# Optimization experiments

Measured on AMD Instinct MI355X. Metric: run time of the kernel, lower is better.

## Reference

```python
import jax, jax.numpy as jnp
import numpy as np

HEADS = 4
BN_EPS = 1e-5


def _linear_attention(x, heads):
    # x: [B, L, C]; per-head linear attention: softmax(Q,dim=feat) @ (softmax(K,dim=seq)^T @ V)
    B, L, C = x.shape
    dh = C // heads
    h = x.reshape(B, L, heads, dh)
    q = jax.nn.softmax(h, axis=-1)          # softmax over feature dim (dim=2 in torch)
    k = jax.nn.softmax(h, axis=1)           # softmax over sequence dim (dim=1 in torch)
    kv = jnp.einsum('blhd,blhe->bhde', k, h)   # [B, H, dh, dh]
    out = jnp.einsum('blhd,bhde->blhe', q, kv) # [B, L, H, dh]
    return out.reshape(B, L, C)


def setup_inputs() -> dict:
    key = jax.random.key(0)
    ks = jax.random.split(key, 10)
    B, C, L, DOUT, NB = 32, 32, 16384, 10, 3
    s = 0.1
    return {
        'x': jax.random.normal(ks[0], (B, C, L), jnp.float32),
        'fcW1': jax.random.normal(ks[1], (NB, C, C), jnp.float32) * s,
        'fcb1': jax.random.normal(ks[2], (NB, C), jnp.float32) * s,
        'fcW2': jax.random.normal(ks[3], (NB, C, C), jnp.float32) * s,
        'fcb2': jax.random.normal(ks[4], (NB, C), jnp.float32) * s,
        'Wh': jax.random.normal(ks[5], (C, C), jnp.float32) * s,
        'bh': jax.random.normal(ks[6], (C,), jnp.float32) * s,
        'bn_gamma': jnp.ones((C,), jnp.float32),
        'bn_beta': jnp.zeros((C,), jnp.float32),
        'bn_mean': jnp.zeros((C,), jnp.float32),
        'bn_var': jnp.ones((C,), jnp.float32),
        'Wf': jax.random.normal(ks[7], (C, DOUT), jnp.float32) * s,
        'bf': jax.random.normal(ks[8], (DOUT,), jnp.float32) * s,
    }


def reference(x, fcW1, fcb1, fcW2, fcb2, Wh, bh, bn_gamma, bn_beta, bn_mean, bn_var, Wf, bf):
    gelu = lambda t: jax.nn.gelu(t, approximate=False)  # torch default GELU is exact erf
    h = jnp.transpose(x, (0, 2, 1))  # [B, C, L] -> [B, L, C]
    n_blocks = fcW1.shape[0]
    for i in range(n_blocks):
        h = _linear_attention(h, HEADS)
        h = gelu(h @ fcW1[i] + fcb1[i])
        h = gelu(h @ fcW2[i] + fcb2[i])
    pooled = jnp.mean(h, axis=1)  # AdaptiveAvgPool1d(1) over L -> [B, C]
    y = pooled @ Wh + bh
    y = (y - bn_mean) * jax.lax.rsqrt(bn_var + BN_EPS) * bn_gamma + bn_beta  # BatchNorm1d (eval)
    y = gelu(y)
    return y @ Wf + bf
```

## Files before the change

### kernel.cpp

```cpp
#include <hip/hip_runtime.h>
#include <cstddef>

#define B_ 32
#define C_ 32
#define L_ 16384
#define H_ 4
#define DH_ 8
#define NB_ 3
#define DOUT_ 10
#define SEG_ 512
#define S_ (L_/SEG_)

#define TILE 256
#define AST  40
#define OST  260

typedef _Float16 f16_t;
typedef _Float16 f16x2 __attribute__((ext_vector_type(2)));
typedef _Float16 f16x8 __attribute__((ext_vector_type(8)));
typedef float    f32x4 __attribute__((ext_vector_type(4)));

__device__ __forceinline__ float gelu_f(float x){
    const float z  = fabsf(x) * 0.70710678118654752440f;
    const float t  = __builtin_amdgcn_rcpf(fmaf(0.3275911f, z, 1.0f));
    const float e  = __expf(-z * z);
    float p = fmaf(t, 1.061405429f, -1.453152027f);
    p = fmaf(t, p, 1.421413741f);
    p = fmaf(t, p, -0.284496736f);
    p = fmaf(t, p, 0.254829592f);
    const float erfz = 1.0f - p * t * e;
    const float phi  = fmaf(copysignf(erfz, x), 0.5f, 0.5f);
    return x * phi;
}

#define RED_MAX32(v) do{ v = fmaxf(v, __shfl_xor(v,1));  v = fmaxf(v, __shfl_xor(v,2)); \
                         v = fmaxf(v, __shfl_xor(v,4));  v = fmaxf(v, __shfl_xor(v,8)); \
                         v = fmaxf(v, __shfl_xor(v,16)); }while(0)
#define RED_SUM32(v) do{ v += __shfl_xor(v,1);  v += __shfl_xor(v,2); \
                         v += __shfl_xor(v,4);  v += __shfl_xor(v,8); \
                         v += __shfl_xor(v,16); }while(0)

__global__ __launch_bounds__(256) void stats_kernel(const float* __restrict__ h,
                                                    float* __restrict__ part){
    const int seg = blockIdx.x;
    const int hd  = blockIdx.y;
    const int b   = blockIdx.z;
    const int t   = threadIdx.x;
    const int d   = t >> 5;
    const int j   = t & 31;

    __shared__ float tile[8][SEG_];
    __shared__ float sm[8];

    const float* hb = h + (size_t)b * ((size_t)C_*L_) + (size_t)(hd*DH_)*L_ + (size_t)seg*SEG_;

    for (int f = t; f < 8*SEG_/4; f += 256){
        const int row = f >> 7;
        const int c4  = (f & 127) << 2;
        *(f32x4*)&tile[row][c4] = *(const f32x4*)&hb[(size_t)row*L_ + c4];
    }
    __syncthreads();

    float m = -INFINITY;
    #pragma unroll
    for (int i = 0; i < SEG_/32; i++) m = fmaxf(m, tile[d][j + 32*i]);
    RED_MAX32(m);
    if (j == 0) sm[d] = m;
    const float m_d = m;

    float s = 0.0f;
    float kv[8];
    #pragma unroll
    for (int e = 0; e < 8; e++) kv[e] = 0.0f;
    #pragma unroll
    for (int i = 0; i < SEG_/32; i++){
        const int k = j + 32*i;
        const float ek = __expf(tile[d][k] - m_d);
        s += ek;
        #pragma unroll
        for (int e = 0; e < 8; e++) kv[e] = fmaf(ek, tile[e][k], kv[e]);
    }
    RED_SUM32(s);
    #pragma unroll
    for (int e = 0; e < 8; e++){ RED_SUM32(kv[e]); }
    __syncthreads();

    float* po = part + (size_t)((b*H_ + hd)*S_ + seg) * 80;
    if (j == 0){
        po[8 + d] = s;
        #pragma unroll
        for (int e = 0; e < 8; e++) po[16 + d*8 + e] = kv[e];
    }
    if (t < 8) po[t] = sm[t];
}

template<bool LAST>
__global__ __launch_bounds__(256)
__attribute__((amdgpu_waves_per_eu(3, 4)))
void block_kernel(const float* hin,
                  float* hout,
                  const float* __restrict__ part,
                  const float* __restrict__ W1,
                  const float* __restrict__ b1,
                  const float* __restrict__ W2,
                  const float* __restrict__ b2,
                  float* __restrict__ pooled){
    __shared__ __align__(16) char AObuf[TILE*AST*2];
    f16_t* const Ash = (f16_t*)AObuf;
    float* const O16 = (float*)AObuf;
    __shared__ f16_t Bsh1[32*AST];
    __shared__ f16_t Bsh2[32*AST];
    __shared__ float sb1[32], sb2[32];
    __shared__ float kvsh[256];
    __shared__ float pool[32];

    const int tid = threadIdx.x;
    const int b   = blockIdx.y;
    const int l0  = blockIdx.x * TILE;
    const int l   = l0 + tid;
    const size_t base = (size_t)b * ((size_t)C_*L_);

    float h[32];
    #pragma unroll
    for (int c = 0; c < 32; c++) h[c] = hin[base + (size_t)c*L_ + l];

    for (int i = tid; i < 1024; i += 256){
        const int k = i >> 5, n = i & 31;
        Bsh1[n*AST + k] = (f16_t)W1[i];
        Bsh2[n*AST + k] = (f16_t)W2[i];
    }
    if (tid < 32){ sb1[tid] = b1[tid]; sb2[tid] = b2[tid]; }
    if (LAST && tid < 32) pool[tid] = 0.0f;

    {
        const int hh_t = tid >> 6;
        const int tt   = tid & 63;
        const int dd   = tt >> 3;
        const float* pp = part + (size_t)(b*H_ + hh_t) * S_ * 80;
        float M = -INFINITY;
        for (int s2 = 0; s2 < S_; s2++) M = fmaxf(M, pp[s2*80 + dd]);
        float ssum = 0.0f, kvs = 0.0f;
        for (int s2 = 0; s2 < S_; s2++){
            const float sc = __expf(pp[s2*80 + dd] - M);
            ssum = fmaf(pp[s2*80 + 8  + dd], sc, ssum);
            kvs  = fmaf(pp[s2*80 + 16 + tt], sc, kvs);
        }
        kvsh[tid] = kvs / ssum;
    }
    __syncthreads();

    float attn[32];
    #pragma unroll
    for (int hh = 0; hh < 4; hh++){
        float mq = h[hh*8];
        #pragma unroll
        for (int d2 = 1; d2 < 8; d2++) mq = fmaxf(mq, h[hh*8 + d2]);
        float es[8]; float qs = 0.f;
        #pragma unroll
        for (int d2 = 0; d2 < 8; d2++){ es[d2] = __expf(h[hh*8 + d2] - mq); qs += es[d2]; }
        const float inv = __builtin_amdgcn_rcpf(qs);
        #pragma unroll
        for (int e = 0; e < 8; e++){
            float a = 0.f;
            #pragma unroll
            for (int d2 = 0; d2 < 8; d2++) a += es[d2] * kvsh[hh*64 + d2*8 + e];
            attn[hh*8 + e] = a * inv;
        }
    }

    #pragma unroll
    for (int k2 = 0; k2 < 32; k2 += 2){
        f16x2 pr = { (f16_t)attn[k2], (f16_t)attn[k2+1] };
        *(f16x2*)&Ash[tid*AST + k2] = pr;
    }
    __syncthreads();

    const int wv   = tid >> 6;
    const int lane = tid & 63;
    const int lr   = lane & 15;
    const int lk   = lane >> 4;
    const f32x4 zero = {0.f, 0.f, 0.f, 0.f};

    f16x8 a[4], bw[2];
    f32x4 d[8];

    #pragma unroll
    for (int mt = 0; mt < 4; mt++)
        a[mt] = *(const f16x8*)&Ash[(wv*64 + mt*16 + lr)*AST + lk*8];
    #pragma unroll
    for (int nt = 0; nt < 2; nt++)
        bw[nt] = *(const f16x8*)&Bsh1[(nt*16 + lr)*AST + lk*8];
    #pragma unroll
    for (int nt = 0; nt < 2; nt++)
        #pragma unroll
        for (int mt = 0; mt < 4; mt++)
            d[nt*4+mt] = __builtin_amdgcn_mfma_f32_16x16x32_f16(a[mt], bw[nt], zero, 0, 0, 0);

    #pragma unroll
    for (int nt = 0; nt < 2; nt++){
        const float bias = sb1[nt*16 + lr];
        #pragma unroll
        for (int mt = 0; mt < 4; mt++){
            #pragma unroll
            for (int r = 0; r < 4; r++){
                const float v = gelu_f(d[nt*4+mt][r] + bias);
                Ash[(wv*64 + mt*16 + lk*4 + r)*AST + (nt*16 + lr)] = (f16_t)v;
            }
        }
    }
    __syncthreads();

    #pragma unroll
    for (int mt = 0; mt < 4; mt++)
        a[mt] = *(const f16x8*)&Ash[(wv*64 + mt*16 + lr)*AST + lk*8];
    #pragma unroll
    for (int nt = 0; nt < 2; nt++)
        bw[nt] = *(const f16x8*)&Bsh2[(nt*16 + lr)*AST + lk*8];
    #pragma unroll
    for (int nt = 0; nt < 2; nt++)
        #pragma unroll
        for (int mt = 0; mt < 4; mt++)
            d[nt*4+mt] = __builtin_amdgcn_mfma_f32_16x16x32_f16(a[mt], bw[nt], zero, 0, 0, 0);

    #pragma unroll
    for (int nt = 0; nt < 2; nt++){
        const float bias = sb2[nt*16 + lr];
        #pragma unroll
        for (int mt = 0; mt < 4; mt++)
            #pragma unroll
            for (int r = 0; r < 4; r++)
                d[nt*4+mt][r] = gelu_f(d[nt*4+mt][r] + bias);
    }

    if (!LAST){
        #pragma unroll
        for (int nt = 0; nt < 2; nt++){
            __syncthreads();
            #pragma unroll
            for (int mt = 0; mt < 4; mt++)
                *(f32x4*)&O16[lr*OST + wv*64 + mt*16 + lk*4] = d[nt*4+mt];
            __syncthreads();
            #pragma unroll
            for (int c = 0; c < 16; c++)
                hout[base + (size_t)(nt*16 + c)*L_ + l0 + tid] = O16[c*OST + tid];
        }
    } else {
        __syncthreads();
        #pragma unroll
        for (int nt = 0; nt < 2; nt++){
            float ps = 0.f;
            #pragma unroll
            for (int mt = 0; mt < 4; mt++)
                ps += d[nt*4+mt][0] + d[nt*4+mt][1] + d[nt*4+mt][2] + d[nt*4+mt][3];
            atomicAdd(&pool[nt*16 + lr], ps);
        }
        __syncthreads();
        if (tid < 32) atomicAdd(&pooled[b*32 + tid], pool[tid]);
    }
}

__global__ __launch_bounds__(1024) void head_kernel(const float* __restrict__ pooled,
                                                    const float* __restrict__ Wh,
                                                    const float* __restrict__ bh,
                                                    const float* __restrict__ gam,
                                                    const float* __restrict__ bet,
                                                    const float* __restrict__ mean,
                                                    const float* __restrict__ var,
                                                    const float* __restrict__ Wf,
                                                    const float* __restrict__ bf,
                                                    float* __restrict__ out){
    __shared__ float y2[32][32];
    const int t = threadIdx.x;
    const int b = t >> 5, c = t & 31;
    float a = bh[c];
    const float invL = 1.0f / (float)L_;
    #pragma unroll
    for (int d = 0; d < 32; d++) a += (pooled[b*32 + d] * invL) * Wh[d*32 + c];
    a = (a - mean[c]) * rsqrtf(var[c] + 1e-5f) * gam[c] + bet[c];
    y2[b][c] = gelu_f(a);
    __syncthreads();
    if (t < B_*DOUT_){
        const int b2 = t / DOUT_, j = t % DOUT_;
        float r = bf[j];
        #pragma unroll
        for (int c2 = 0; c2 < 32; c2++) r += y2[b2][c2] * Wf[c2*DOUT_ + j];
        out[t] = r;
    }
}

extern "C" void kernel_launch(void* const* d_in, const int* in_sizes, int n_in,
                              void* d_out, int out_size, void* d_ws, size_t ws_size,
                              hipStream_t stream){
    (void)in_sizes; (void)n_in; (void)out_size; (void)ws_size;
    const float* x    = (const float*)d_in[0];
    const float* fW1  = (const float*)d_in[1];
    const float* fb1  = (const float*)d_in[2];
    const float* fW2  = (const float*)d_in[3];
    const float* fb2  = (const float*)d_in[4];
    const float* Wh   = (const float*)d_in[5];
    const float* bh   = (const float*)d_in[6];
    const float* gam  = (const float*)d_in[7];
    const float* bet  = (const float*)d_in[8];
    const float* mean = (const float*)d_in[9];
    const float* var  = (const float*)d_in[10];
    const float* Wf   = (const float*)d_in[11];
    const float* bf   = (const float*)d_in[12];
    float* out = (float*)d_out;

    float* hbuf   = (float*)d_ws;
    float* part   = hbuf + (size_t)B_*C_*L_;
    float* pooled = part + (size_t)B_*H_*S_*80;

    hipMemsetAsync(pooled, 0, B_*C_*sizeof(float), stream);

    dim3 sgrid(S_, H_, B_);
    dim3 bgrid(L_/TILE, B_);

    stats_kernel<<<sgrid, 256, 0, stream>>>(x, part);
    block_kernel<false><<<bgrid, 256, 0, stream>>>(x, hbuf, part,
        fW1, fb1, fW2, fb2, nullptr);
    stats_kernel<<<sgrid, 256, 0, stream>>>(hbuf, part);
    block_kernel<false><<<bgrid, 256, 0, stream>>>(hbuf, hbuf, part,
        fW1 + C_*C_, fb1 + C_, fW2 + C_*C_, fb2 + C_, nullptr);
    stats_kernel<<<sgrid, 256, 0, stream>>>(hbuf, part);
    block_kernel<true><<<bgrid, 256, 0, stream>>>(hbuf, nullptr, part,
        fW1 + 2*C_*C_, fb1 + 2*C_, fW2 + 2*C_*C_, fb2 + 2*C_, pooled);

    head_kernel<<<1, 1024, 0, stream>>>(pooled, Wh, bh, gam, bet, mean, var, Wf, bf, out);
}
```

Baseline: 294.1 us.

## Process two sub-tiles per block, store MFMA output directly, fuse head into last block

Each block now covers 512 sequence positions as two 256-wide sub-tiles, with both input slices loaded into registers up front so the second load overlaps the first sub-tile's compute. The output no longer goes through an LDS transpose: 16-byte vectors are written straight from the MFMA accumulators to global memory. The separate head kernel is folded into the last block kernel, using a global completion counter and threadfences so the final block computes the head. This saves a launch and several barriers, but raises register pressure and makes the global stores less coalesced.

```diff
diff --git a/kernel.cpp b/kernel.cpp
--- a/kernel.cpp
+++ b/kernel.cpp
@@ -11,9 +11,8 @@
 #define SEG_ 512
 #define S_ (L_/SEG_)
 
-#define TILE 256
+#define WTILE 512
 #define AST  40
-#define OST  260
 
 typedef _Float16 f16_t;
 typedef _Float16 f16x2 __attribute__((ext_vector_type(2)));
@@ -104,25 +103,35 @@
                   const float* __restrict__ b1,
                   const float* __restrict__ W2,
                   const float* __restrict__ b2,
-                  float* __restrict__ pooled){
-    __shared__ __align__(16) char AObuf[TILE*AST*2];
-    f16_t* const Ash = (f16_t*)AObuf;
-    float* const O16 = (float*)AObuf;
+                  float* pooled,
+                  unsigned* done_ctr,
+                  const float* __restrict__ Wh,
+                  const float* __restrict__ bh,
+                  const float* __restrict__ gam,
+                  const float* __restrict__ bet,
+                  const float* __restrict__ mean,
+                  const float* __restrict__ var,
+                  const float* __restrict__ Wf,
+                  const float* __restrict__ bf,
+                  float* __restrict__ out){
+    __shared__ __align__(16) f16_t Ash[256*AST];
     __shared__ f16_t Bsh1[32*AST];
     __shared__ f16_t Bsh2[32*AST];
     __shared__ float sb1[32], sb2[32];
     __shared__ float kvsh[256];
     __shared__ float pool[32];
+    __shared__ unsigned lastf;
 
     const int tid = threadIdx.x;
     const int b   = blockIdx.y;
-    const int l0  = blockIdx.x * TILE;
-    const int l   = l0 + tid;
+    const int l0  = blockIdx.x * WTILE;
     const size_t base = (size_t)b * ((size_t)C_*L_);
 
-    float h[32];
-    #pragma unroll
-    for (int c = 0; c < 32; c++) h[c] = hin[base + (size_t)c*L_ + l];
+    float h0[32], h1[32];
+    #pragma unroll
+    for (int c = 0; c < 32; c++) h0[c] = hin[base + (size_t)c*L_ + l0 + tid];
+    #pragma unroll
+    for (int c = 0; c < 32; c++) h1[c] = hin[base + (size_t)c*L_ + l0 + 256 + tid];
 
     for (int i = tid; i < 1024; i += 256){
         const int k = i >> 5, n = i & 31;
@@ -149,142 +158,148 @@
     }
     __syncthreads();
 
-    float attn[32];
-    #pragma unroll
-    for (int hh = 0; hh < 4; hh++){
-        float mq = h[hh*8];
-        #pragma unroll
-        for (int d2 = 1; d2 < 8; d2++) mq = fmaxf(mq, h[hh*8 + d2]);
-        float es[8]; float qs = 0.f;
-        #pragma unroll
-        for (int d2 = 0; d2 < 8; d2++){ es[d2] = __expf(h[hh*8 + d2] - mq); qs += es[d2]; }
-        const float inv = __builtin_amdgcn_rcpf(qs);
-        #pragma unroll
-        for (int e = 0; e < 8; e++){
-            float a = 0.f;
-            #pragma unroll
-            for (int d2 = 0; d2 < 8; d2++) a += es[d2] * kvsh[hh*64 + d2*8 + e];
-            attn[hh*8 + e] = a * inv;
-        }
-    }
-
-    #pragma unroll
-    for (int k2 = 0; k2 < 32; k2 += 2){
-        f16x2 pr = { (f16_t)attn[k2], (f16_t)attn[k2+1] };
-        *(f16x2*)&Ash[tid*AST + k2] = pr;
-    }
-    __syncthreads();
-
     const int wv   = tid >> 6;
     const int lane = tid & 63;
     const int lr   = lane & 15;
     const int lk   = lane >> 4;
     const f32x4 zero = {0.f, 0.f, 0.f, 0.f};
 
-    f16x8 a[4], bw[2];
-    f32x4 d[8];
-
-    #pragma unroll
-    for (int mt = 0; mt < 4; mt++)
-        a[mt] = *(const f16x8*)&Ash[(wv*64 + mt*16 + lr)*AST + lk*8];
-    #pragma unroll
-    for (int nt = 0; nt < 2; nt++)
-        bw[nt] = *(const f16x8*)&Bsh1[(nt*16 + lr)*AST + lk*8];
-    #pragma unroll
-    for (int nt = 0; nt < 2; nt++)
+    auto attn_to_ash = [&](const float (&hh)[32], const bool preb){
+        float attn[32];
+        #pragma unroll
+        for (int hd2 = 0; hd2 < 4; hd2++){
+            float mq = hh[hd2*8];
+            #pragma unroll
+            for (int d2 = 1; d2 < 8; d2++) mq = fmaxf(mq, hh[hd2*8 + d2]);
+            float es[8]; float qs = 0.f;
+            #pragma unroll
+            for (int d2 = 0; d2 < 8; d2++){ es[d2] = __expf(hh[hd2*8 + d2] - mq); qs += es[d2]; }
+            const float inv = __builtin_amdgcn_rcpf(qs);
+            #pragma unroll
+            for (int e = 0; e < 8; e++){
+                float acc = 0.f;
+                #pragma unroll
+                for (int d2 = 0; d2 < 8; d2++) acc += es[d2] * kvsh[hd2*64 + d2*8 + e];
+                attn[hd2*8 + e] = acc * inv;
+            }
+        }
+        if (preb) __syncthreads();
+        #pragma unroll
+        for (int k2 = 0; k2 < 32; k2 += 2){
+            f16x2 pr = { (f16_t)attn[k2], (f16_t)attn[k2+1] };
+            *(f16x2*)&Ash[tid*AST + k2] = pr;
+        }
+    };
+
+    auto fc_and_out = [&](const int lofs){
+        f16x8 a[4], bw[2];
+        f32x4 d[8];
         #pragma unroll
         for (int mt = 0; mt < 4; mt++)
-            d[nt*4+mt] = __builtin_amdgcn_mfma_f32_16x16x32_f16(a[mt], bw[nt], zero, 0, 0, 0);
-
-    #pragma unroll
-    for (int nt = 0; nt < 2; nt++){
-        const float bias = sb1[nt*16 + lr];
-        #pragma unroll
-        for (int mt = 0; mt < 4; mt++){
-            #pragma unroll
-            for (int r = 0; r < 4; r++){
-                const float v = gelu_f(d[nt*4+mt][r] + bias);
-                Ash[(wv*64 + mt*16 + lk*4 + r)*AST + (nt*16 + lr)] = (f16_t)v;
+            a[mt] = *(const f16x8*)&Ash[(wv*64 + mt*16 + lr)*AST + lk*8];
+        #pragma unroll
+        for (int nt = 0; nt < 2; nt++)
+            bw[nt] = *(const f16x8*)&Bsh1[(nt*16 + lr)*AST + lk*8];
+        #pragma unroll
+        for (int nt = 0; nt < 2; nt++)
+            #pragma unroll
+            for (int mt = 0; mt < 4; mt++)
+                d[nt*4+mt] = __builtin_amdgcn_mfma_f32_16x16x32_f16(a[mt], bw[nt], zero, 0, 0, 0);
+
+        #pragma unroll
+        for (int nt = 0; nt < 2; nt++){
+            const float bias = sb1[nt*16 + lr];
+            #pragma unroll
+            for (int mt = 0; mt < 4; mt++)
+                #pragma unroll
+                for (int r = 0; r < 4; r++){
+                    const float v = gelu_f(d[nt*4+mt][r] + bias);
+                    Ash[(wv*64 + mt*16 + lk*4 + r)*AST + (nt*16 + lr)] = (f16_t)v;
+                }
+        }
+
+        #pragma unroll
+        for (int mt = 0; mt < 4; mt++)
+            a[mt] = *(const f16x8*)&Ash[(wv*64 + mt*16 + lr)*AST + lk*8];
+        #pragma unroll
+        for (int nt = 0; nt < 2; nt++)
+            bw[nt] = *(const f16x8*)&Bsh2[(nt*16 + lr)*AST + lk*8];
+        #pragma unroll
+        for (int nt = 0; nt < 2; nt++)
+            #pragma unroll
+            for (int mt = 0; mt < 4; mt++)
+                d[nt*4+mt] = __builtin_amdgcn_mfma_f32_16x16x32_f16(a[mt], bw[nt], zero, 0, 0, 0);
+
+        #pragma unroll
+        for (int nt = 0; nt < 2; nt++){
+            const float bias = sb2[nt*16 + lr];
+            #pragma unroll
+            for (int mt = 0; mt < 4; mt++)
+                #pragma unroll
+                for (int r = 0; r < 4; r++)
+                    d[nt*4+mt][r] = gelu_f(d[nt*4+mt][r] + bias);
+        }
+
+        if (!LAST){
+            #pragma unroll
+            for (int nt = 0; nt < 2; nt++)
+                #pragma unroll
+                for (int mt = 0; mt < 4; mt++)
+                    *(f32x4*)&hout[base + (size_t)(nt*16 + lr)*L_
+                                   + l0 + lofs + wv*64 + mt*16 + lk*4] = d[nt*4+mt];
+        } else {
+            #pragma unroll
+            for (int nt = 0; nt < 2; nt++){
+                float ps = 0.f;
+                #pragma unroll
+                for (int mt = 0; mt < 4; mt++)
+                    ps += d[nt*4+mt][0] + d[nt*4+mt][1] + d[nt*4+mt][2] + d[nt*4+mt][3];
+                atomicAdd(&pool[nt*16 + lr], ps);
             }
         }
-    }
-    __syncthreads();
-
-    #pragma unroll
-    for (int mt = 0; mt < 4; mt++)
-        a[mt] = *(const f16x8*)&Ash[(wv*64 + mt*16 + lr)*AST + lk*8];
-    #pragma unroll
-    for (int nt = 0; nt < 2; nt++)
-        bw[nt] = *(const f16x8*)&Bsh2[(nt*16 + lr)*AST + lk*8];
-    #pragma unroll
-    for (int nt = 0; nt < 2; nt++)
-        #pragma unroll
-        for (int mt = 0; mt < 4; mt++)
-            d[nt*4+mt] = __builtin_amdgcn_mfma_f32_16x16x32_f16(a[mt], bw[nt], zero, 0, 0, 0);
-
-    #pragma unroll
-    for (int nt = 0; nt < 2; nt++){
-        const float bias = sb2[nt*16 + lr];
-        #pragma unroll
-        for (int mt = 0; mt < 4; mt++)
-            #pragma unroll
-            for (int r = 0; r < 4; r++)
-                d[nt*4+mt][r] = gelu_f(d[nt*4+mt][r] + bias);
-    }
-
-    if (!LAST){
-        #pragma unroll
-        for (int nt = 0; nt < 2; nt++){
+    };
+
+    attn_to_ash(h0, false);
+    __syncthreads();
+    fc_and_out(0);
+    attn_to_ash(h1, true);
+    __syncthreads();
+    fc_and_out(256);
+
+    if (LAST){
+        __syncthreads();
+        if (tid < 32){
+            atomicAdd(&pooled[b*32 + tid], pool[tid]);
+            __threadfence();
+        }
+        __syncthreads();
+        if (tid == 0){
+            const unsigned old = atomicAdd(done_ctr, 1u);
+            lastf = (old == 1023u) ? 1u : 0u;
+        }
+        __syncthreads();
+        if (lastf){
+            __threadfence();
+            float* y2 = (float*)Ash;
+            const float invL = 1.0f / (float)L_;
+            for (int i = tid; i < 1024; i += 256){
+                const int bb = i >> 5, cc = i & 31;
+                float acc = bh[cc];
+                #pragma unroll
+                for (int dd2 = 0; dd2 < 32; dd2++)
+                    acc += (pooled[bb*32 + dd2] * invL) * Wh[dd2*32 + cc];
+                acc = (acc - mean[cc]) * rsqrtf(var[cc] + 1e-5f) * gam[cc] + bet[cc];
+                y2[i] = gelu_f(acc);
+            }
             __syncthreads();
-            #pragma unroll
-            for (int mt = 0; mt < 4; mt++)
-                *(f32x4*)&O16[lr*OST + wv*64 + mt*16 + lk*4] = d[nt*4+mt];
-            __syncthreads();
-            #pragma unroll
-            for (int c = 0; c < 16; c++)
-                hout[base + (size_t)(nt*16 + c)*L_ + l0 + tid] = O16[c*OST + tid];
-        }
-    } else {
-        __syncthreads();
-        #pragma unroll
-        for (int nt = 0; nt < 2; nt++){
-            float ps = 0.f;
-            #pragma unroll
-            for (int mt = 0; mt < 4; mt++)
-                ps += d[nt*4+mt][0] + d[nt*4+mt][1] + d[nt*4+mt][2] + d[nt*4+mt][3];
-            atomicAdd(&pool[nt*16 + lr], ps);
-        }
-        __syncthreads();
-        if (tid < 32) atomicAdd(&pooled[b*32 + tid], pool[tid]);
-    }
-}
-
-__global__ __launch_bounds__(1024) void head_kernel(const float* __restrict__ pooled,
-                                                    const float* __restrict__ Wh,
-                                                    const float* __restrict__ bh,
-                                                    const float* __restrict__ gam,
-                                                    const float* __restrict__ bet,
-                                                    const float* __restrict__ mean,
-                                                    const float* __restrict__ var,
-                                                    const float* __restrict__ Wf,
-                                                    const float* __restrict__ bf,
-                                                    float* __restrict__ out){
-    __shared__ float y2[32][32];
-    const int t = threadIdx.x;
-    const int b = t >> 5, c = t & 31;
-    float a = bh[c];
-    const float invL = 1.0f / (float)L_;
-    #pragma unroll
-    for (int d = 0; d < 32; d++) a += (pooled[b*32 + d] * invL) * Wh[d*32 + c];
-    a = (a - mean[c]) * rsqrtf(var[c] + 1e-5f) * gam[c] + bet[c];
-    y2[b][c] = gelu_f(a);
-    __syncthreads();
-    if (t < B_*DOUT_){
-        const int b2 = t / DOUT_, j = t % DOUT_;
-        float r = bf[j];
-        #pragma unroll
-        for (int c2 = 0; c2 < 32; c2++) r += y2[b2][c2] * Wf[c2*DOUT_ + j];
-        out[t] = r;
+            for (int i = tid; i < B_*DOUT_; i += 256){
+                const int b2 = i / DOUT_, j = i % DOUT_;
+                float r = bf[j];
+                #pragma unroll
+                for (int c2 = 0; c2 < 32; c2++) r += y2[b2*32 + c2] * Wf[c2*DOUT_ + j];
+                out[i] = r;
+            }
+        }
     }
 }
 
@@ -307,24 +322,26 @@
     const float* bf   = (const float*)d_in[12];
     float* out = (float*)d_out;
 
-    float* hbuf   = (float*)d_ws;
-    float* part   = hbuf + (size_t)B_*C_*L_;
-    float* pooled = part + (size_t)B_*H_*S_*80;
-
-    hipMemsetAsync(pooled, 0, B_*C_*sizeof(float), stream);
+    float* hbuf    = (float*)d_ws;
+    float* part    = hbuf + (size_t)B_*C_*L_;
+    float* pooled  = part + (size_t)B_*H_*S_*80;
+    unsigned* done = (unsigned*)(pooled + B_*C_);
+
+    hipMemsetAsync(pooled, 0, (B_*C_ + 1)*sizeof(float), stream);
 
     dim3 sgrid(S_, H_, B_);
-    dim3 bgrid(L_/TILE, B_);
+    dim3 bgrid(L_/WTILE, B_);
 
     stats_kernel<<<sgrid, 256, 0, stream>>>(x, part);
     block_kernel<false><<<bgrid, 256, 0, stream>>>(x, hbuf, part,
-        fW1, fb1, fW2, fb2, nullptr);
+        fW1, fb1, fW2, fb2, nullptr, nullptr,
+        nullptr, nullptr, nullptr, nullptr, nullptr, nullptr, nullptr, nullptr, nullptr);
     stats_kernel<<<sgrid, 256, 0, stream>>>(hbuf, part);
     block_kernel<false><<<bgrid, 256, 0, stream>>>(hbuf, hbuf, part,
-        fW1 + C_*C_, fb1 + C_, fW2 + C_*C_, fb2 + C_, nullptr);
+        fW1 + C_*C_, fb1 + C_, fW2 + C_*C_, fb2 + C_, nullptr, nullptr,
+        nullptr, nullptr, nullptr, nullptr, nullptr, nullptr, nullptr, nullptr, nullptr);
     stats_kernel<<<sgrid, 256, 0, stream>>>(hbuf, part);
     block_kernel<true><<<bgrid, 256, 0, stream>>>(hbuf, nullptr, part,
-        fW1 + 2*C_*C_, fb1 + 2*C_, fW2 + 2*C_*C_, fb2 + 2*C_, pooled);
-
-    head_kernel<<<1, 1024, 0, stream>>>(pooled, Wh, bh, gam, bet, mean, var, Wf, bf, out);
+        fW1 + 2*C_*C_, fb1 + 2*C_, fW2 + 2*C_*C_, fb2 + 2*C_, pooled, done,
+        Wh, bh, gam, bet, mean, var, Wf, bf, out);
 }
```

Result: slower. 303.1 us (+3.1%).
